# Performance work log

Measured on AMD Instinct MI355X. Metric: run time of the kernel, lower is better.

Reference implementation:

```python
import jax, jax.numpy as jnp
import numpy as np

N_NODES = 20000
N_EDGES = 320000
F_IN = 256
HID = 256
N_CLS = 5


def _glorot(key, shape):
    lim = np.sqrt(6.0 / (shape[0] + shape[1]))
    return jax.random.uniform(key, shape, jnp.float32, -lim, lim)


def setup_inputs() -> dict:
    key = jax.random.key(0)
    ks = jax.random.split(key, 12)
    x1 = jax.random.normal(ks[0], (N_NODES, F_IN), jnp.float32)
    x2 = jax.random.normal(ks[1], (N_NODES, F_IN), jnp.float32)
    ei1 = jax.random.randint(ks[2], (2, N_EDGES), 0, N_NODES, jnp.int64 if jax.config.jax_enable_x64 else jnp.int32)
    ei2 = jax.random.randint(ks[3], (2, N_EDGES), 0, N_NODES, jnp.int64 if jax.config.jax_enable_x64 else jnp.int32)
    params = {
        'W1': _glorot(ks[4], (F_IN, HID)), 'b1': jnp.zeros((HID,), jnp.float32),
        'W2': _glorot(ks[5], (HID, HID)), 'b2': jnp.zeros((HID,), jnp.float32),
        'W3': _glorot(ks[6], (HID, HID)), 'b3': jnp.zeros((HID,), jnp.float32),
        'Wl': _glorot(ks[7], (HID, N_CLS)), 'bl': jnp.zeros((N_CLS,), jnp.float32),
    }
    return {'x1': x1, 'edge_index1': ei1, 'x2': x2, 'edge_index2': ei2, **params}


def gcn_conv(x, edge_index, W, b):
    # PyG GCNConv: add self-loops, symmetric normalization D^-1/2 (A+I) D^-1/2 (X W) + b
    N = x.shape[0]
    src, dst = edge_index[0], edge_index[1]
    deg = jax.ops.segment_sum(jnp.ones(src.shape[0], x.dtype), dst, num_segments=N) + 1.0
    dinv = jax.lax.rsqrt(deg)  # [N]
    xw = x @ W                 # [N, H]
    coef = (dinv[src] * dinv[dst])[:, None]  # per-edge norm
    agg = jax.ops.segment_sum(xw[src] * coef, dst, num_segments=N)
    agg = agg + xw * (dinv * dinv)[:, None]  # self-loop term
    return agg + b


def _branch(x, ei, W1, b1, W2, b2, W3, b3):
    # dropout is identity in eval mode
    h = jax.nn.relu(gcn_conv(x, ei, W1, b1))
    h = jax.nn.relu(gcn_conv(h, ei, W2, b2))
    return gcn_conv(h, ei, W3, b3)


def reference(x1, edge_index1, x2, edge_index2, W1, b1, W2, b2, W3, b3, Wl, bl):
    h1 = _branch(x1, edge_index1, W1, b1, W2, b2, W3, b3)
    h2 = _branch(x2, edge_index2, W1, b1, W2, b2, W3, b3)
    h = jnp.concatenate([h1, h2], axis=0)          # [2N, H]
    pooled = jnp.mean(h, axis=0, keepdims=True)    # batch is all zeros -> single mean pool
    return pooled @ Wl + bl                        # [1, num_classes]
```

## Files before the change

### kernel.cpp

```cpp
#include <hip/hip_runtime.h>
#include <hip/hip_bf16.h>

#define N_NODES 20000
#define N_EDGES 320000
#define HID 256
#define NQ 5000
#define NCHUNK 64

typedef __attribute__((ext_vector_type(8))) short bf16x8;
typedef __attribute__((ext_vector_type(4))) float f32x4;
typedef __attribute__((ext_vector_type(8))) unsigned short us8;

__device__ __forceinline__ float bf2f(ushort u) {
  union { unsigned int i; float f; } v; v.i = ((unsigned int)u) << 16; return v.f;
}
__device__ __forceinline__ ushort f2bf(float f) {
  union { float f; unsigned int i; } v; v.f = f;
  unsigned int r = v.i + 0x7FFFu + ((v.i >> 16) & 1u);
  return (ushort)(r >> 16);
}

__global__ void init_detect_kernel(int* cnt0, int* cnt1, float* t0, float* t1,
                                   const void* x1, const void* ei1, int* flags) {
  if (blockIdx.x == gridDim.x - 1) {
    __shared__ int cnt_wild, cnt_oddnz;
    if (threadIdx.x == 0) { cnt_wild = 0; cnt_oddnz = 0; }
    __syncthreads();
    const ushort* xu = (const ushort*)x1;
    int wild = 0;
#pragma unroll
    for (int k = 0; k < 4; k++) {
      ushort u = xu[threadIdx.x * 4 + k];
      int ex = (u >> 7) & 0xFF;
      if (ex >= 0x90) wild++;
    }
    if (wild) atomicAdd(&cnt_wild, wild);
    const int* ii = (const int*)ei1;
    if (ii[threadIdx.x * 2 + 1] != 0) atomicAdd(&cnt_oddnz, 1);
    __syncthreads();
    if (threadIdx.x == 0) {
      flags[0] = (cnt_wild > 64) ? 1 : 0;
      flags[1] = (cnt_oddnz < 8) ? 1 : 0;
    }
    return;
  }
  int i = blockIdx.x * blockDim.x + threadIdx.x;
  if (i < N_NODES) { cnt0[i] = 0; cnt1[i] = 0; t0[i] = 0.f; t1[i] = 0.f; }
}

__global__ __launch_bounds__(256) void wt_kernel(
    const void* __restrict__ W1, const void* __restrict__ W2,
    ushort* __restrict__ Wt1, ushort* __restrict__ Wt2,
    const int* __restrict__ flags) {
  bool f32 = flags[0] != 0;
  int which = blockIdx.x >> 8;
  int k = blockIdx.x & 255;
  const void* W = which ? W2 : W1;
  ushort* Wt = which ? Wt2 : Wt1;
  int n = threadIdx.x;
  ushort v = f32 ? f2bf(((const float*)W)[k * 256 + n])
                 : ((const ushort*)W)[k * 256 + n];
  Wt[n * 256 + k] = v;
}

__global__ __launch_bounds__(512) void count_rank_kernel(
    const void* e0, const void* e1, int* cnt0, int* cnt1,
    int* rank0, int* rank1, const int* flags) {
  int b = blockIdx.y;
  const void* e = b ? e1 : e0;
  int* cnt = b ? cnt1 : cnt0;
  int* rank = b ? rank1 : rank0;
  int chunk = blockIdx.x >> 2;
  int lo = (blockIdx.x & 3) * NQ;
  int ebeg = chunk * (N_EDGES / NCHUNK);
  int eend = ebeg + (N_EDGES / NCHUNK);
  __shared__ int hist[NQ];
  __shared__ int base[NQ];
  for (int k = threadIdx.x; k < NQ; k += 512) hist[k] = 0;
  __syncthreads();
  bool w64 = flags[1] != 0;
  const int* d32 = (const int*)e + N_EDGES;
  const long long* d64 = (const long long*)e + N_EDGES;
  for (int i = ebeg + threadIdx.x; i < eend; i += 512) {
    int d = w64 ? (int)d64[i] : d32[i];
    unsigned q = (unsigned)(d - lo);
    if (q < NQ) atomicAdd(&hist[q], 1);
  }
  __syncthreads();
  for (int k = threadIdx.x; k < NQ; k += 512) {
    int h = hist[k];
    if (h) base[k] = atomicAdd(&cnt[lo + k], h);
    hist[k] = 0;
  }
  __syncthreads();
  for (int i = ebeg + threadIdx.x; i < eend; i += 512) {
    int d = w64 ? (int)d64[i] : d32[i];
    unsigned q = (unsigned)(d - lo);
    if (q < NQ) rank[i] = base[q] + atomicAdd(&hist[q], 1);
  }
}

__global__ __launch_bounds__(1024) void scan_kernel(const int* cnt0, const int* cnt1,
                                                    int* rp0, int* rp1,
                                                    float* dinv0, float* dinv1) {
  const int* cnt = blockIdx.x ? cnt1 : cnt0;
  int* rp = blockIdx.x ? rp1 : rp0;
  float* dinv = blockIdx.x ? dinv1 : dinv0;
  __shared__ int sd[1024];
  int tid = threadIdx.x;
  int base = tid * 20;
  int pref[20];
  int run = 0;
#pragma unroll
  for (int k = 0; k < 20; k++) {
    int i = base + k;
    int c = (i < N_NODES) ? cnt[i] : 0;
    if (i < N_NODES) dinv[i] = rsqrtf((float)c + 1.0f);
    run += c;
    pref[k] = run;
  }
  sd[tid] = run;
  __syncthreads();
  for (int off = 1; off < 1024; off <<= 1) {
    int v = (tid >= off) ? sd[tid - off] : 0;
    __syncthreads();
    sd[tid] += v;
    __syncthreads();
  }
  int offset = sd[tid] - run;
  if (tid == 0) rp[0] = 0;
#pragma unroll
  for (int k = 0; k < 20; k++) {
    int i = base + k;
    if (i < N_NODES) rp[i + 1] = offset + pref[k];
  }
}

__global__ __launch_bounds__(512) void fill_kernel(
    const void* e0, const void* e1,
    const float* dinv0, const float* dinv1,
    const int* rp0, const int* rp1,
    const int* rank0, const int* rank1,
    unsigned int* eg0, unsigned int* eg1,
    float* t0, float* t1, const int* flags) {
  int b = blockIdx.y;
  const void* e = b ? e1 : e0;
  const float* dinv = b ? dinv1 : dinv0;
  bool w64 = flags[1] != 0;
  const int* s32 = (const int*)e;
  const int* d32 = (const int*)e + N_EDGES;
  const long long* s64 = (const long long*)e;
  const long long* d64 = (const long long*)e + N_EDGES;
  if (blockIdx.x < 625) {
    const int* rp = b ? rp1 : rp0;
    const int* rank = b ? rank1 : rank0;
    unsigned int* eg = b ? eg1 : eg0;
    int i = blockIdx.x * 512 + threadIdx.x;
    int src = w64 ? (int)s64[i] : s32[i];
    int dst = w64 ? (int)d64[i] : d32[i];
    int slot = rp[dst] + rank[i];
    eg[slot] = (unsigned int)src | ((unsigned int)f2bf(dinv[src] * dinv[dst]) << 16);
    return;
  }
  float* t = b ? t1 : t0;
  int r = blockIdx.x - 625;
  int chunk = r >> 2;
  int lo = (r & 3) * NQ;
  int ebeg = chunk * (N_EDGES / NCHUNK);
  int eend = ebeg + (N_EDGES / NCHUNK);
  __shared__ float tl[NQ];
  for (int k = threadIdx.x; k < NQ; k += 512) tl[k] = 0.f;
  __syncthreads();
  for (int i = ebeg + threadIdx.x; i < eend; i += 512) {
    int src = w64 ? (int)s64[i] : s32[i];
    unsigned q = (unsigned)(src - lo);
    if (q < NQ) {
      int dst = w64 ? (int)d64[i] : d32[i];
      atomicAdd(&tl[q], dinv[dst]);
    }
  }
  __syncthreads();
  for (int k = threadIdx.x; k < NQ; k += 512) {
    float v = tl[k];
    if (v != 0.f) atomicAdd(&t[lo + k], v);
  }
}

__global__ __launch_bounds__(256) void gemm_kernel(
    const void* __restrict__ A0, const void* __restrict__ A1,
    const ushort* __restrict__ Wt,
    ushort* __restrict__ C0, ushort* __restrict__ C1,
    int maybe_f32, const int* __restrict__ flags) {
  const void* A = blockIdx.z ? A1 : A0;
  ushort* C = blockIdx.z ? C1 : C0;
  bool af32 = maybe_f32 && (flags[0] != 0);
  int m0 = blockIdx.x * 32;
  __shared__ __align__(16) ushort As[32][264];
  int tid = threadIdx.x;
  int wave = tid >> 6, lane = tid & 63;
  int quad = lane >> 4, r16 = lane & 15;
  int nb = wave * 64;
  {
    int row = tid >> 3, c0 = (tid & 7) * 32;
    int gr = m0 + row;
    if (af32) {
      const float* pA = (const float*)A + gr * 256 + c0;
      ushort* d = &As[row][c0];
#pragma unroll
      for (int s = 0; s < 8; s++) {
        float4 v = *(const float4*)(pA + s * 4);
        d[s * 4 + 0] = f2bf(v.x); d[s * 4 + 1] = f2bf(v.y);
        d[s * 4 + 2] = f2bf(v.z); d[s * 4 + 3] = f2bf(v.w);
      }
    } else {
      const ushort* pA = (const ushort*)A + gr * 256 + c0;
#pragma unroll
      for (int s = 0; s < 4; s++)
        *(int4*)&As[row][c0 + s * 8] = *(const int4*)(pA + s * 8);
    }
  }
  __syncthreads();
  f32x4 acc[2][4];
#pragma unroll
  for (int m = 0; m < 2; m++)
#pragma unroll
    for (int n = 0; n < 4; n++) acc[m][n] = (f32x4){0.f, 0.f, 0.f, 0.f};
#pragma unroll
  for (int k0 = 0; k0 < 256; k0 += 32) {
    bf16x8 a0 = *(const bf16x8*)&As[r16][k0 + quad * 8];
    bf16x8 a1 = *(const bf16x8*)&As[16 + r16][k0 + quad * 8];
    const ushort* wp = Wt + (nb + r16) * 256 + k0 + quad * 8;
    bf16x8 bb0 = *(const bf16x8*)(wp);
    bf16x8 bb1 = *(const bf16x8*)(wp + 16 * 256);
    bf16x8 bb2 = *(const bf16x8*)(wp + 32 * 256);
    bf16x8 bb3 = *(const bf16x8*)(wp + 48 * 256);
    acc[0][0] = __builtin_amdgcn_mfma_f32_16x16x32_bf16(a0, bb0, acc[0][0], 0, 0, 0);
    acc[0][1] = __builtin_amdgcn_mfma_f32_16x16x32_bf16(a0, bb1, acc[0][1], 0, 0, 0);
    acc[0][2] = __builtin_amdgcn_mfma_f32_16x16x32_bf16(a0, bb2, acc[0][2], 0, 0, 0);
    acc[0][3] = __builtin_amdgcn_mfma_f32_16x16x32_bf16(a0, bb3, acc[0][3], 0, 0, 0);
    acc[1][0] = __builtin_amdgcn_mfma_f32_16x16x32_bf16(a1, bb0, acc[1][0], 0, 0, 0);
    acc[1][1] = __builtin_amdgcn_mfma_f32_16x16x32_bf16(a1, bb1, acc[1][1], 0, 0, 0);
    acc[1][2] = __builtin_amdgcn_mfma_f32_16x16x32_bf16(a1, bb2, acc[1][2], 0, 0, 0);
    acc[1][3] = __builtin_amdgcn_mfma_f32_16x16x32_bf16(a1, bb3, acc[1][3], 0, 0, 0);
  }
#pragma unroll
  for (int m = 0; m < 2; m++) {
    int grb = m0 + m * 16 + quad * 4;
#pragma unroll
    for (int r = 0; r < 4; r++) {
      int gr = grb + r;
      ushort* cp = C + gr * 256 + nb + r16;
      cp[0]  = f2bf(acc[m][0][r]);
      cp[16] = f2bf(acc[m][1][r]);
      cp[32] = f2bf(acc[m][2][r]);
      cp[48] = f2bf(acc[m][3][r]);
    }
  }
}

__global__ __launch_bounds__(256) void agg_kernel(
    const ushort* __restrict__ XW0, const ushort* __restrict__ XW1,
    const float* __restrict__ dinv0, const float* __restrict__ dinv1,
    const int* __restrict__ rp0, const int* __restrict__ rp1,
    const unsigned int* __restrict__ eg0, const unsigned int* __restrict__ eg1,
    const void* __restrict__ bias,
    ushort* __restrict__ H0, ushort* __restrict__ H1,
    const int* __restrict__ flags) {
  int b = blockIdx.y;
  const ushort* XW = b ? XW1 : XW0;
  const float* dinv = b ? dinv1 : dinv0;
  const int* rp = b ? rp1 : rp0;
  const unsigned int* eg = b ? eg1 : eg0;
  ushort* H = b ? H1 : H0;
  int wave = threadIdx.x >> 6, lane = threadIdx.x & 63;
  int grp = lane >> 3;
  int fo = (lane & 7) * 8 + blockIdx.z * 64;
  int i = blockIdx.x * 32 + wave * 8 + grp;
  float di = dinv[i];
  float selfw = di * di;
  us8 v = *(const us8*)(XW + i * 256 + fo);
  float acc[8], acc2[8];
#pragma unroll
  for (int k = 0; k < 8; k++) { acc[k] = selfw * bf2f(v[k]); acc2[k] = 0.f; }
  int e = rp[i], eend = rp[i + 1];
  for (; e + 4 <= eend; e += 4) {
    unsigned int p0 = eg[e], p1 = eg[e + 1], p2 = eg[e + 2], p3 = eg[e + 3];
    us8 r0 = *(const us8*)(XW + (p0 & 0xFFFFu) * 256 + fo);
    us8 r1 = *(const us8*)(XW + (p1 & 0xFFFFu) * 256 + fo);
    us8 r2 = *(const us8*)(XW + (p2 & 0xFFFFu) * 256 + fo);
    us8 r3 = *(const us8*)(XW + (p3 & 0xFFFFu) * 256 + fo);
    float w0 = bf2f((ushort)(p0 >> 16)), w1 = bf2f((ushort)(p1 >> 16));
    float w2 = bf2f((ushort)(p2 >> 16)), w3 = bf2f((ushort)(p3 >> 16));
#pragma unroll
    for (int k = 0; k < 8; k++) {
      acc[k]  += w0 * bf2f(r0[k]);
      acc2[k] += w1 * bf2f(r1[k]);
      acc[k]  += w2 * bf2f(r2[k]);
      acc2[k] += w3 * bf2f(r3[k]);
    }
  }
  for (; e < eend; e++) {
    unsigned int pp = eg[e];
    us8 r = *(const us8*)(XW + (pp & 0xFFFFu) * 256 + fo);
    float w = bf2f((ushort)(pp >> 16));
#pragma unroll
    for (int k = 0; k < 8; k++) acc[k] += w * bf2f(r[k]);
  }
  float bv[8];
  if (flags[0]) {
    const float* bf = (const float*)bias + fo;
    float4 c0 = *(const float4*)bf;
    float4 c1 = *(const float4*)(bf + 4);
    bv[0] = c0.x; bv[1] = c0.y; bv[2] = c0.z; bv[3] = c0.w;
    bv[4] = c1.x; bv[5] = c1.y; bv[6] = c1.z; bv[7] = c1.w;
  } else {
    us8 bb = *(const us8*)((const ushort*)bias + fo);
#pragma unroll
    for (int k = 0; k < 8; k++) bv[k] = bf2f(bb[k]);
  }
  us8 o;
#pragma unroll
  for (int k = 0; k < 8; k++)
    o[k] = f2bf(fmaxf(acc[k] + acc2[k] + bv[k], 0.f));
  *(us8*)(H + i * 256 + fo) = o;
}

__global__ __launch_bounds__(256) void colsum_kernel(
    const ushort* __restrict__ H0, const ushort* __restrict__ H1,
    const float* __restrict__ dinv0, const float* __restrict__ dinv1,
    const float* __restrict__ t0, const float* __restrict__ t1,
    float* __restrict__ P) {
  int b = blockIdx.y;
  const ushort* H = b ? H1 : H0;
  const float* dinv = b ? dinv1 : dinv0;
  const float* t = b ? t1 : t0;
  int wave = threadIdx.x >> 6, lane = threadIdx.x & 63;
  int wid = blockIdx.x * 4 + wave;
  int f4 = lane * 4;
  float a0 = 0.f, a1 = 0.f, a2 = 0.f, a3 = 0.f;
  for (int j = wid; j < N_NODES; j += 256) {
    float dj = dinv[j];
    float c = dj * (t[j] + dj);
    ushort4 u = *(const ushort4*)(H + j * 256 + f4);
    a0 += c * bf2f(u.x); a1 += c * bf2f(u.y);
    a2 += c * bf2f(u.z); a3 += c * bf2f(u.w);
  }
  __shared__ float part[4][256];
  part[wave][f4 + 0] = a0; part[wave][f4 + 1] = a1;
  part[wave][f4 + 2] = a2; part[wave][f4 + 3] = a3;
  __syncthreads();
  int f = threadIdx.x;
  float ssum = part[0][f] + part[1][f] + part[2][f] + part[3][f];
  P[(b * 64 + blockIdx.x) * 256 + f] = ssum;
}

__global__ __launch_bounds__(256) void final_kernel(
    const float* __restrict__ P,
    const void* __restrict__ W3, const void* __restrict__ b3,
    const void* __restrict__ Wl, const void* __restrict__ bl,
    void* __restrict__ out, const int* __restrict__ flags) {
  __shared__ float v[256];
  __shared__ float pooled[256];
  bool f32 = flags[0] != 0;
  int t = threadIdx.x;
  float acc0 = 0.f, acc1 = 0.f;
  for (int b = 0; b < 64; b++) {
    acc0 += P[b * 256 + t];
    acc1 += P[(64 + b) * 256 + t];
  }
  v[t] = acc0 + acc1;
  __syncthreads();
  float acc = 0.f;
  if (f32) {
    const float* W3f = (const float*)W3;
    for (int f = 0; f < 256; f++) acc += v[f] * W3f[f * 256 + t];
    pooled[t] = acc * (1.0f / (2.0f * N_NODES)) + ((const float*)b3)[t];
  } else {
    const ushort* W3b = (const ushort*)W3;
    for (int f = 0; f < 256; f++) acc += v[f] * bf2f(W3b[f * 256 + t]);
    pooled[t] = acc * (1.0f / (2.0f * N_NODES)) + bf2f(((const ushort*)b3)[t]);
  }
  __syncthreads();
  if (t < 5) {
    float o;
    if (f32) {
      o = ((const float*)bl)[t];
      for (int h = 0; h < 256; h++) o += pooled[h] * ((const float*)Wl)[h * 5 + t];
      ((float*)out)[t] = o;
    } else {
      o = bf2f(((const ushort*)bl)[t]);
      for (int h = 0; h < 256; h++) o += pooled[h] * bf2f(((const ushort*)Wl)[h * 5 + t]);
      ((ushort*)out)[t] = f2bf(o);
    }
  }
}

extern "C" void kernel_launch(void* const* d_in, const int* in_sizes, int n_in,
                              void* d_out, int out_size, void* d_ws, size_t ws_size,
                              hipStream_t stream) {
  const void* x1 = d_in[0];
  const void* ei1 = d_in[1];
  const void* x2 = d_in[2];
  const void* ei2 = d_in[3];
  const void* W1 = d_in[4];
  const void* b1 = d_in[5];
  const void* W2 = d_in[6];
  const void* b2 = d_in[7];
  const void* W3 = d_in[8];
  const void* b3 = d_in[9];
  const void* Wl = d_in[10];
  const void* bl = d_in[11];

  char* p = (char*)d_ws;
  auto alloc = [&](size_t bytes) {
    char* r = p;
    p += (bytes + 255) & ~size_t(255);
    return r;
  };
  int* flags   = (int*)alloc(256);
  float* dinv0 = (float*)alloc(N_NODES * 4);
  float* dinv1 = (float*)alloc(N_NODES * 4);
  float* t0    = (float*)alloc(N_NODES * 4);
  float* t1    = (float*)alloc(N_NODES * 4);
  int* cnt0    = (int*)alloc(N_NODES * 4);
  int* cnt1    = (int*)alloc(N_NODES * 4);
  int* rp0     = (int*)alloc((N_NODES + 1) * 4);
  int* rp1     = (int*)alloc((N_NODES + 1) * 4);
  unsigned int* eg0 = (unsigned int*)alloc((size_t)N_EDGES * 4);
  unsigned int* eg1 = (unsigned int*)alloc((size_t)N_EDGES * 4);
  float* Pp    = (float*)alloc(2 * 64 * 256 * 4);
  ushort* wt1  = (ushort*)alloc(256 * 256 * 2);
  ushort* wt2  = (ushort*)alloc(256 * 256 * 2);
  ushort* xw0  = (ushort*)alloc((size_t)N_NODES * HID * 2);
  ushort* xw1  = (ushort*)alloc((size_t)N_NODES * HID * 2);
  ushort* h0   = (ushort*)alloc((size_t)N_NODES * HID * 2);
  ushort* h1   = (ushort*)alloc((size_t)N_NODES * HID * 2);
  int* rank0  = (int*)xw0;
  int* rank1  = rank0 + N_EDGES;

  init_detect_kernel<<<(N_NODES + 255) / 256 + 1, 256, 0, stream>>>(
      cnt0, cnt1, t0, t1, x1, ei1, flags);
  wt_kernel<<<512, 256, 0, stream>>>(W1, W2, wt1, wt2, flags);
  count_rank_kernel<<<dim3(NCHUNK * 4, 2), 512, 0, stream>>>(
      ei1, ei2, cnt0, cnt1, rank0, rank1, flags);
  scan_kernel<<<2, 1024, 0, stream>>>(cnt0, cnt1, rp0, rp1, dinv0, dinv1);
  fill_kernel<<<dim3(625 + NCHUNK * 4, 2), 512, 0, stream>>>(
      ei1, ei2, dinv0, dinv1, rp0, rp1, rank0, rank1, eg0, eg1, t0, t1, flags);

  gemm_kernel<<<dim3(625, 1, 2), 256, 0, stream>>>(x1, x2, wt1, xw0, xw1, 1, flags);
  agg_kernel<<<dim3(625, 2, 4), 256, 0, stream>>>(
      xw0, xw1, dinv0, dinv1, rp0, rp1, eg0, eg1, b1, h0, h1, flags);

  gemm_kernel<<<dim3(625, 1, 2), 256, 0, stream>>>(h0, h1, wt2, xw0, xw1, 0, flags);
  agg_kernel<<<dim3(625, 2, 4), 256, 0, stream>>>(
      xw0, xw1, dinv0, dinv1, rp0, rp1, eg0, eg1, b2, h0, h1, flags);

  colsum_kernel<<<dim3(64, 2), 256, 0, stream>>>(h0, h1, dinv0, dinv1, t0, t1, Pp);
  final_kernel<<<1, 256, 0, stream>>>(Pp, W3, b3, Wl, bl, d_out, flags);
}
```

Measured before the change: 360.8 us.

## Fuse first-layer GEMM into edge count/rank kernel to run concurrently

Merges the layer-1 X·W1 GEMM and the edge-destination counting/ranking pass into a single heterogeneous launch. Block indices select either GEMM tiles or count/rank work, and the two roles share one static shared-memory buffer. The rank scratch buffer moves from xw0 to h0 so the concurrently written GEMM output does not alias it. This removes one kernel launch and lets the compute-bound GEMM overlap the atomic-heavy counting pass, at the cost of larger shared-memory use and 512-thread blocks for the GEMM role.

Result: faster. 351.2 us (-2.7%).

```diff
diff --git a/kernel.cpp b/kernel.cpp
--- a/kernel.cpp
+++ b/kernel.cpp
@@ -63,19 +63,102 @@
   Wt[n * 256 + k] = v;
 }
 
-__global__ __launch_bounds__(512) void count_rank_kernel(
+__global__ __launch_bounds__(512) void countgemm_kernel(
     const void* e0, const void* e1, int* cnt0, int* cnt1,
-    int* rank0, int* rank1, const int* flags) {
-  int b = blockIdx.y;
+    int* rank0, int* rank1,
+    const void* __restrict__ A0, const void* __restrict__ A1,
+    const ushort* __restrict__ Wt,
+    ushort* __restrict__ C0, ushort* __restrict__ C1,
+    const int* __restrict__ flags) {
+  __shared__ __align__(16) char smem[40960];
+  if (blockIdx.x < 626) {
+    int g = blockIdx.x;
+    int br = (g >= 313) ? 1 : 0;
+    int tile = g - 313 * br;
+    const void* A = br ? A1 : A0;
+    ushort* C = br ? C1 : C0;
+    bool af32 = flags[0] != 0;
+    int unit = threadIdx.x >> 8;
+    int t = threadIdx.x & 255;
+    int m0 = tile * 64 + unit * 32;
+    ushort (*As)[264] = reinterpret_cast<ushort(*)[264]>(smem + unit * 16896);
+    int wave = t >> 6, lane = t & 63;
+    int quad = lane >> 4, r16 = lane & 15;
+    int nb = wave * 64;
+    {
+      int row = t >> 3, c0 = (t & 7) * 32;
+      int gr = m0 + row;
+      if (gr < N_NODES) {
+        if (af32) {
+          const float* pA = (const float*)A + gr * 256 + c0;
+          ushort* d = &As[row][c0];
+#pragma unroll
+          for (int s = 0; s < 8; s++) {
+            float4 v = *(const float4*)(pA + s * 4);
+            d[s * 4 + 0] = f2bf(v.x); d[s * 4 + 1] = f2bf(v.y);
+            d[s * 4 + 2] = f2bf(v.z); d[s * 4 + 3] = f2bf(v.w);
+          }
+        } else {
+          const ushort* pA = (const ushort*)A + gr * 256 + c0;
+#pragma unroll
+          for (int s = 0; s < 4; s++)
+            *(int4*)&As[row][c0 + s * 8] = *(const int4*)(pA + s * 8);
+        }
+      }
+    }
+    __syncthreads();
+    f32x4 acc[2][4];
+#pragma unroll
+    for (int m = 0; m < 2; m++)
+#pragma unroll
+      for (int n = 0; n < 4; n++) acc[m][n] = (f32x4){0.f, 0.f, 0.f, 0.f};
+#pragma unroll
+    for (int k0 = 0; k0 < 256; k0 += 32) {
+      bf16x8 a0 = *(const bf16x8*)&As[r16][k0 + quad * 8];
+      bf16x8 a1 = *(const bf16x8*)&As[16 + r16][k0 + quad * 8];
+      const ushort* wp = Wt + (nb + r16) * 256 + k0 + quad * 8;
+      bf16x8 bb0 = *(const bf16x8*)(wp);
+      bf16x8 bb1 = *(const bf16x8*)(wp + 16 * 256);
+      bf16x8 bb2 = *(const bf16x8*)(wp + 32 * 256);
+      bf16x8 bb3 = *(const bf16x8*)(wp + 48 * 256);
+      acc[0][0] = __builtin_amdgcn_mfma_f32_16x16x32_bf16(a0, bb0, acc[0][0], 0, 0, 0);
+      acc[0][1] = __builtin_amdgcn_mfma_f32_16x16x32_bf16(a0, bb1, acc[0][1], 0, 0, 0);
+      acc[0][2] = __builtin_amdgcn_mfma_f32_16x16x32_bf16(a0, bb2, acc[0][2], 0, 0, 0);
+      acc[0][3] = __builtin_amdgcn_mfma_f32_16x16x32_bf16(a0, bb3, acc[0][3], 0, 0, 0);
+      acc[1][0] = __builtin_amdgcn_mfma_f32_16x16x32_bf16(a1, bb0, acc[1][0], 0, 0, 0);
+      acc[1][1] = __builtin_amdgcn_mfma_f32_16x16x32_bf16(a1, bb1, acc[1][1], 0, 0, 0);
+      acc[1][2] = __builtin_amdgcn_mfma_f32_16x16x32_bf16(a1, bb2, acc[1][2], 0, 0, 0);
+      acc[1][3] = __builtin_amdgcn_mfma_f32_16x16x32_bf16(a1, bb3, acc[1][3], 0, 0, 0);
+    }
+#pragma unroll
+    for (int m = 0; m < 2; m++) {
+      int grb = m0 + m * 16 + quad * 4;
+#pragma unroll
+      for (int r = 0; r < 4; r++) {
+        int gr = grb + r;
+        if (gr < N_NODES) {
+          ushort* cp = C + gr * 256 + nb + r16;
+          cp[0]  = f2bf(acc[m][0][r]);
+          cp[16] = f2bf(acc[m][1][r]);
+          cp[32] = f2bf(acc[m][2][r]);
+          cp[48] = f2bf(acc[m][3][r]);
+        }
+      }
+    }
+    return;
+  }
+  int cb = blockIdx.x - 626;
+  int b = cb >> 8;
+  int x = cb & 255;
   const void* e = b ? e1 : e0;
   int* cnt = b ? cnt1 : cnt0;
   int* rank = b ? rank1 : rank0;
-  int chunk = blockIdx.x >> 2;
-  int lo = (blockIdx.x & 3) * NQ;
+  int chunk = x >> 2;
+  int lo = (x & 3) * NQ;
   int ebeg = chunk * (N_EDGES / NCHUNK);
   int eend = ebeg + (N_EDGES / NCHUNK);
-  __shared__ int hist[NQ];
-  __shared__ int base[NQ];
+  int* hist = (int*)smem;
+  int* base = hist + NQ;
   for (int k = threadIdx.x; k < NQ; k += 512) hist[k] = 0;
   __syncthreads();
   bool w64 = flags[1] != 0;
@@ -435,19 +518,21 @@
   ushort* xw1  = (ushort*)alloc((size_t)N_NODES * HID * 2);
   ushort* h0   = (ushort*)alloc((size_t)N_NODES * HID * 2);
   ushort* h1   = (ushort*)alloc((size_t)N_NODES * HID * 2);
-  int* rank0  = (int*)xw0;
+  int* rank0  = (int*)h0;
   int* rank1  = rank0 + N_EDGES;
 
   init_detect_kernel<<<(N_NODES + 255) / 256 + 1, 256, 0, stream>>>(
       cnt0, cnt1, t0, t1, x1, ei1, flags);
   wt_kernel<<<512, 256, 0, stream>>>(W1, W2, wt1, wt2, flags);
-  count_rank_kernel<<<dim3(NCHUNK * 4, 2), 512, 0, stream>>>(
-      ei1, ei2, cnt0, cnt1, rank0, rank1, flags);
+
+  countgemm_kernel<<<626 + 512, 512, 0, stream>>>(
+      ei1, ei2, cnt0, cnt1, rank0, rank1,
+      x1, x2, wt1, xw0, xw1, flags);
+
   scan_kernel<<<2, 1024, 0, stream>>>(cnt0, cnt1, rp0, rp1, dinv0, dinv1);
   fill_kernel<<<dim3(625 + NCHUNK * 4, 2), 512, 0, stream>>>(
       ei1, ei2, dinv0, dinv1, rp0, rp1, rank0, rank1, eg0, eg1, t0, t1, flags);
 
-  gemm_kernel<<<dim3(625, 1, 2), 256, 0, stream>>>(x1, x2, wt1, xw0, xw1, 1, flags);
   agg_kernel<<<dim3(625, 2, 4), 256, 0, stream>>>(
       xw0, xw1, dinv0, dinv1, rp0, rp1, eg0, eg1, b1, h0, h1, flags);
 
```
